# Kernel optimization log

Hardware: AMD Instinct MI355X
Metric: run time of the kernel (lower is better)

Reference implementation:

```python
import jax, jax.numpy as jnp
import numpy as np

N = 200_000   # nodes per component
E = 400_000   # directed edges per component
F_IN = 32     # raw node features
H = 96        # hidden_dim / GatedGraphConv out_channels
L = 6         # num_layers inside GatedGraphConv
B = 4096      # number of molecules (graphs) in batch
FC = 4 * H    # 384


def _gru_cell(m, h, w_ih, w_hh, b_ih, b_hh):
    # torch.nn.GRUCell math; w_* are [3H, H], b_* are [3H]
    gi = m @ w_ih.T + b_ih
    gh = h @ w_hh.T + b_hh
    i_r, i_z, i_n = jnp.split(gi, 3, axis=1)
    h_r, h_z, h_n = jnp.split(gh, 3, axis=1)
    r = jax.nn.sigmoid(i_r + h_r)
    z = jax.nn.sigmoid(i_z + h_z)
    n = jnp.tanh(i_n + r * h_n)
    return (1.0 - z) * n + z * h


def _gated_graph_conv(x, edge_index, W, w_ih, w_hh, b_ih, b_hh):
    n_nodes = x.shape[0]
    h = jnp.pad(x, ((0, 0), (0, H - x.shape[1])))  # pad features to H
    src, dst = edge_index[0], edge_index[1]        # message flows src -> dst
    for i in range(L):
        m = h @ W[i]                                # [N, H]
        agg = jax.ops.segment_sum(m[src], dst, num_segments=n_nodes)
        h = _gru_cell(agg, h, w_ih, w_hh, b_ih, b_hh)
    return h


def _pool_component(x, edge_index, batch, W, w_ih, w_hh, b_ih, b_hh):
    h = jax.nn.relu(_gated_graph_conv(x, edge_index, W, w_ih, w_hh, b_ih, b_hh))
    sums = jax.ops.segment_sum(h, batch, num_segments=B)
    cnt = jax.ops.segment_sum(jnp.ones((h.shape[0], 1), h.dtype), batch, num_segments=B)
    return sums / jnp.maximum(cnt, 1.0)            # global_mean_pool -> [B, H]


def setup_inputs() -> dict:
    key = jax.random.key(0)
    ks = jax.random.split(key, 16)
    d = {}
    for i in range(3):
        c = str(i + 1)
        kx, ke, kb = jax.random.split(ks[i], 3)
        d['x' + c] = jax.random.normal(kx, (N, F_IN), jnp.float32)
        d['edge_index' + c] = jax.random.randint(ke, (2, E), 0, N)
        d['batch' + c] = jnp.sort(jax.random.randint(kb, (N,), 0, B))
        kw = jax.random.split(ks[3 + i], 5)
        d['W' + c] = jax.random.normal(kw[0], (L, H, H), jnp.float32) * 0.05
        d['wih' + c] = jax.random.normal(kw[1], (3 * H, H), jnp.float32) * 0.05
        d['whh' + c] = jax.random.normal(kw[2], (3 * H, H), jnp.float32) * 0.05
        d['bih' + c] = jax.random.normal(kw[3], (3 * H,), jnp.float32) * 0.05
        d['bhh' + c] = jax.random.normal(kw[4], (3 * H,), jnp.float32) * 0.05
    kf = jax.random.split(ks[7], 6)
    d['fc1_w'] = jax.random.normal(kf[0], (FC, FC * 4), jnp.float32) * 0.05
    d['fc1_b'] = jnp.zeros((FC * 4,), jnp.float32)
    d['fc2_w'] = jax.random.normal(kf[1], (FC * 4, FC), jnp.float32) * 0.05
    d['fc2_b'] = jnp.zeros((FC,), jnp.float32)
    d['fc3_w'] = jax.random.normal(kf[2], (FC, 3), jnp.float32) * 0.05
    d['fc3_b'] = jnp.zeros((3,), jnp.float32)
    return d


def reference(x1, edge_index1, batch1, x2, edge_index2, batch2, x3, edge_index3, batch3,
              W1, wih1, whh1, bih1, bhh1,
              W2, wih2, whh2, bih2, bhh2,
              W3, wih3, whh3, bih3, bhh3,
              fc1_w, fc1_b, fc2_w, fc2_b, fc3_w, fc3_b):
    g1 = _pool_component(x1, edge_index1, batch1, W1, wih1, whh1, bih1, bhh1)
    g2 = _pool_component(x2, edge_index2, batch2, W2, wih2, whh2, bih2, bhh2)
    g3 = _pool_component(x3, edge_index3, batch3, W3, wih3, whh3, bih3, bhh3)
    xx = g1 * g2 * g3
    x = jnp.concatenate((g1, g2, g3, xx), axis=1)   # [B, 4H]
    x = jax.nn.relu(x @ fc1_w + fc1_b)              # dropout is identity (eval)
    x = jax.nn.relu(x @ fc2_w + fc2_b)
    return x @ fc3_w + fc3_b                        # [B, 3]
```

## Files before the change

### kernel.cpp

```cpp
#include <hip/hip_runtime.h>
#include <math.h>

#define NN_ 200000
#define EE_ 400000
#define HH  96
#define LL  6
#define BB  4096
#define NT_ 12500
#define SCAN_B 1024
#define NB_SCAN 196

typedef short s8v __attribute__((ext_vector_type(8)));
typedef float f4v __attribute__((ext_vector_type(4)));
typedef float f2v __attribute__((ext_vector_type(2)));

static inline int cdiv(int a, int b) { return (a + b - 1) / b; }

__device__ __forceinline__ float sigmoidf_(float x) { return 1.0f / (1.0f + __expf(-x)); }
__device__ __forceinline__ float tanhf_(float x) { return 1.0f - 2.0f / (__expf(2.0f * x) + 1.0f); }
__device__ __forceinline__ unsigned short f2bf(float x) {
    unsigned u = __float_as_uint(x);
    unsigned r = u + 0x7FFF + ((u >> 16) & 1);
    return (unsigned short)(r >> 16);
}
__device__ __forceinline__ float bf2f(unsigned short u) {
    return __uint_as_float(((unsigned)u) << 16);
}
__device__ __forceinline__ s8v load_bf8(const float* __restrict__ p) {
    float4 v0 = *(const float4*)p;
    float4 v1 = *(const float4*)(p + 4);
    s8v r;
    r[0] = (short)f2bf(v0.x); r[1] = (short)f2bf(v0.y);
    r[2] = (short)f2bf(v0.z); r[3] = (short)f2bf(v0.w);
    r[4] = (short)f2bf(v1.x); r[5] = (short)f2bf(v1.y);
    r[6] = (short)f2bf(v1.z); r[7] = (short)f2bf(v1.w);
    return r;
}

__device__ __forceinline__ void accu_(f2v& a, unsigned u) {
    a[0] += __uint_as_float(u << 16);
    a[1] += __uint_as_float(u & 0xFFFF0000u);
}
__device__ __forceinline__ void acc_row_(f2v* ag2, const uint4& u, int ks) {
    accu_(ag2[ks * 4 + 0], u.x); accu_(ag2[ks * 4 + 1], u.y);
    accu_(ag2[ks * 4 + 2], u.z); accu_(ag2[ks * 4 + 3], u.w);
}

__global__ void packB_k(const float* __restrict__ B, unsigned short* __restrict__ Bp,
                        int K, int N)
{
    int idx = blockIdx.x * 256 + threadIdx.x;
    if (idx >= K * N) return;
    int k = idx / N, n = idx % N;
    Bp[(((size_t)(k >> 5) * N + n) * 4 + ((k >> 3) & 3)) * 8 + (k & 7)] = f2bf(B[idx]);
}

__global__ void packWp_k(const float* __restrict__ W, unsigned short* __restrict__ Wp)
{
    int idx = blockIdx.x * 256 + threadIdx.x;
    if (idx >= LL * 6 * 3 * 64 * 8) return;
    int j    = idx & 7;
    int lane = (idx >> 3) & 63;
    int rest = idx >> 9;
    int ks = rest % 3;
    int jb = (rest / 3) % 6;
    int l  = rest / 18;
    int quad = lane >> 4, lc = lane & 15;
    int k = ks * 32 + quad * 8 + j;
    int n = jb * 16 + lc;
    Wp[idx] = f2bf(W[(size_t)l * 9216 + (size_t)k * 96 + n]);
}

__global__ void packWgc_k(const float* __restrict__ wih, const float* __restrict__ whh,
                          unsigned short* __restrict__ Wgc)
{
    int idx = blockIdx.x * 256 + threadIdx.x;
    if (idx >= 6 * 18 * 64 * 8) return;
    int j    = idx & 7;
    int lane = (idx >> 3) & 63;
    int rest = idx >> 9;
    int ksb = rest % 18;
    int jb  = rest / 18;
    int quad = lane >> 4, lc = lane & 15;
    int g, ks;
    if (ksb < 6)       { g = 0; ks = ksb; }
    else if (ksb < 12) { g = 1; ks = ksb - 6; }
    else if (ksb < 15) { g = 2; ks = ksb - 12; }
    else               { g = 3; ks = ksb - 12; }
    int k = ks * 32 + quad * 8 + j;
    int n = g * 96 + jb * 16 + lc;
    float v;
    if (n < 192) {
        v = (k < 96) ? wih[(size_t)n * 96 + k] : whh[(size_t)n * 96 + (k - 96)];
    } else if (n < 288) {
        int jj = n - 192;
        v = wih[(size_t)(192 + jj) * 96 + k];
    } else {
        int jj = n - 288;
        v = whh[(size_t)(192 + jj) * 96 + (k - 96)];
    }
    Wgc[idx] = f2bf(v);
}

__global__ void bpack_k(const float* __restrict__ bih, const float* __restrict__ bhh,
                        float* __restrict__ bs)
{
    int j = threadIdx.x;
    if (j >= 96) return;
    bs[j]        = bih[j] + bhh[j];
    bs[96 + j]   = bih[96 + j] + bhh[96 + j];
    bs[192 + j]  = bih[192 + j];
    bs[288 + j]  = bhh[192 + j];
}

__global__ void pad_k(const float* __restrict__ x, float* __restrict__ h,
                      unsigned short* __restrict__ hbf)
{
    int idx = blockIdx.x * 256 + threadIdx.x;
    if (idx >= NN_ * HH) return;
    int n = idx / HH, j = idx % HH;
    float v = (j < 32) ? x[n * 32 + j] : 0.f;
    h[idx] = v;
    hbf[idx] = f2bf(v);
}

__global__ void deg_k(const int* __restrict__ ei, int* __restrict__ deg)
{
    int e = blockIdx.x * 256 + threadIdx.x;
    if (e >= EE_) return;
    atomicAdd(&deg[ei[EE_ + e]], 1);
}

__global__ __launch_bounds__(SCAN_B) void scan1_k(
    const int* __restrict__ deg, int* __restrict__ rp, int* __restrict__ bsum)
{
    __shared__ int sh[SCAN_B];
    int i = blockIdx.x * SCAN_B + threadIdx.x;
    int v = (i < NN_) ? deg[i] : 0;
    sh[threadIdx.x] = v;
    __syncthreads();
    for (int off = 1; off < SCAN_B; off <<= 1) {
        int t = (threadIdx.x >= off) ? sh[threadIdx.x - off] : 0;
        __syncthreads();
        sh[threadIdx.x] += t;
        __syncthreads();
    }
    if (i < NN_) rp[i] = sh[threadIdx.x] - v;
    if (threadIdx.x == SCAN_B - 1) bsum[blockIdx.x] = sh[threadIdx.x];
}

__global__ __launch_bounds__(256) void scan2_k(int* __restrict__ bsum)
{
    __shared__ int sh[256];
    int v = (threadIdx.x < NB_SCAN) ? bsum[threadIdx.x] : 0;
    sh[threadIdx.x] = v;
    __syncthreads();
    for (int off = 1; off < 256; off <<= 1) {
        int t = (threadIdx.x >= off) ? sh[threadIdx.x - off] : 0;
        __syncthreads();
        sh[threadIdx.x] += t;
        __syncthreads();
    }
    if (threadIdx.x < NB_SCAN) bsum[threadIdx.x] = sh[threadIdx.x] - v;
}

__global__ void scan3_k(int* __restrict__ rp, const int* __restrict__ bsum,
                        int* __restrict__ cur)
{
    int i = blockIdx.x * 256 + threadIdx.x;
    if (i < NN_) {
        int r = rp[i] + bsum[i / SCAN_B];
        rp[i] = r;
        cur[i] = r;
    }
    if (i == 0) rp[NN_] = EE_;
}

__global__ void fill_k(const int* __restrict__ ei, int* __restrict__ cur,
                       int* __restrict__ srcs)
{
    int e = blockIdx.x * 256 + threadIdx.x;
    if (e >= EE_) return;
    int s = ei[e];
    int d = ei[EE_ + e];
    int pos = atomicAdd(&cur[d], 1);
    srcs[pos] = s * 192;
}

__global__ void brp_k(const int* __restrict__ bat, int* __restrict__ rpb)
{
    int i = blockIdx.x * 256 + threadIdx.x;
    if (i >= NN_) return;
    int b = bat[i];
    if (i == 0) {
        for (int q = 0; q <= b; q++) rpb[q] = 0;
    } else {
        int p = bat[i - 1];
        for (int q = p + 1; q <= b; q++) rpb[q] = i;
    }
    if (i == NN_ - 1) {
        for (int q = b + 1; q <= BB; q++) rpb[q] = NN_;
    }
}

__global__ __launch_bounds__(128) void agg_k(
    const int* __restrict__ rp, const int* __restrict__ srcs,
    const unsigned short* __restrict__ hbf,
    unsigned short* __restrict__ aggbf)
{
    int tid  = threadIdx.x;
    int wave = tid >> 6;
    int lane = tid & 63;
    int quad = lane >> 4;
    int lc   = lane & 15;
    int nT0  = blockIdx.x * 4 + wave * 2;

    const char* gbase = (const char*)hbf + quad * 16;

    #pragma unroll
    for (int t = 0; t < 2; t++) {
        int node = (nT0 + t) * 16 + lc;
        f2v ag2[12];
        #pragma unroll
        for (int i = 0; i < 12; i++) ag2[i] = (f2v){0.f, 0.f};
        int e = rp[node], e1 = rp[node + 1];
        for (; e < e1; e++) {
            const char* r = gbase + srcs[e];
            uint4 u0 = *(const uint4*)r;
            uint4 u1 = *(const uint4*)(r + 64);
            uint4 u2 = *(const uint4*)(r + 128);
            acc_row_(ag2, u0, 0); acc_row_(ag2, u1, 1); acc_row_(ag2, u2, 2);
        }
        #pragma unroll
        for (int ks = 0; ks < 3; ks++) {
            unsigned q0 = (unsigned)f2bf(ag2[ks * 4 + 0][0]) | ((unsigned)f2bf(ag2[ks * 4 + 0][1]) << 16);
            unsigned q1 = (unsigned)f2bf(ag2[ks * 4 + 1][0]) | ((unsigned)f2bf(ag2[ks * 4 + 1][1]) << 16);
            unsigned q2 = (unsigned)f2bf(ag2[ks * 4 + 2][0]) | ((unsigned)f2bf(ag2[ks * 4 + 2][1]) << 16);
            unsigned q3 = (unsigned)f2bf(ag2[ks * 4 + 3][0]) | ((unsigned)f2bf(ag2[ks * 4 + 3][1]) << 16);
            *(uint4*)(aggbf + (size_t)node * 96 + ks * 32 + quad * 8) =
                make_uint4(q0, q1, q2, q3);
        }
    }
}

__global__ __launch_bounds__(512, 2) void gru_k(
    const unsigned short* __restrict__ aggbf,
    const unsigned short* __restrict__ Wp,
    const unsigned short* __restrict__ Wgc,
    const float* __restrict__ bs,
    float* __restrict__ h,
    unsigned short* __restrict__ hbf)
{
    __shared__ unsigned short lw[55296];
    __shared__ unsigned short as_[8][32][36];
    int tid = threadIdx.x;

    {
        const uint4* src = (const uint4*)Wgc;
        uint4* dst = (uint4*)lw;
        #pragma unroll
        for (int it = 0; it < 14; it++) {
            int i = it * 512 + tid;
            if (i < 6912) dst[i] = src[i];
        }
    }
    __syncthreads();

    int wave = tid >> 6;
    int lane = tid & 63;
    int quad = lane >> 4;
    int lc   = lane & 15;
    int nT0  = blockIdx.x * 16 + wave * 2;

    bool val[2];
    val[0] = (nT0 + 0) < NT_;
    val[1] = (nT0 + 1) < NT_;

    s8v z8;
    #pragma unroll
    for (int q = 0; q < 8; q++) z8[q] = 0;

    s8v hg[2][3], dh[2][3];
    #pragma unroll
    for (int t = 0; t < 2; t++) {
        int node = (nT0 + t) * 16 + lc;
        #pragma unroll
        for (int ks = 0; ks < 3; ks++) {
            if (val[t]) {
                hg[t][ks] = *(const s8v*)(aggbf + (size_t)node * 96 + ks * 32 + quad * 8);
                dh[t][ks] = *(const s8v*)(hbf   + (size_t)node * 96 + ks * 32 + quad * 8);
            } else {
                hg[t][ks] = z8;
                dh[t][ks] = z8;
            }
        }
    }

    s8v d[2][6];
    #pragma unroll
    for (int kb = 0; kb < 3; kb++) {
        #pragma unroll
        for (int jj = 0; jj < 2; jj++) {
            int jb = kb * 2 + jj;
            f4v a1[2] = {};
            #pragma unroll
            for (int ks = 0; ks < 3; ks++) {
                s8v w = *(const s8v*)(Wp + ((size_t)(jb * 3 + ks) * 64 + lane) * 8);
                a1[0] = __builtin_amdgcn_mfma_f32_16x16x32_bf16(w, hg[0][ks], a1[0], 0, 0, 0);
                a1[1] = __builtin_amdgcn_mfma_f32_16x16x32_bf16(w, hg[1][ks], a1[1], 0, 0, 0);
            }
            #pragma unroll
            for (int t = 0; t < 2; t++) {
                unsigned short o0 = f2bf(a1[t][0]), o1 = f2bf(a1[t][1]);
                unsigned short o2 = f2bf(a1[t][2]), o3 = f2bf(a1[t][3]);
                *(uint2*)&as_[wave][t * 16 + lc][jj * 16 + quad * 4] =
                    make_uint2((unsigned)o0 | ((unsigned)o1 << 16),
                               (unsigned)o2 | ((unsigned)o3 << 16));
            }
        }
        #pragma unroll
        for (int t = 0; t < 2; t++)
            d[t][kb] = *(const s8v*)&as_[wave][t * 16 + lc][quad * 8];
    }
    #pragma unroll
    for (int t = 0; t < 2; t++) {
        d[t][3] = dh[t][0]; d[t][4] = dh[t][1]; d[t][5] = dh[t][2];
    }

    for (int jb = 0; jb < 6; jb++) {
        float4 hold[2];
        #pragma unroll
        for (int t = 0; t < 2; t++) {
            if (val[t])
                hold[t] = *(const float4*)(h + (size_t)((nT0 + t) * 16 + lc) * 96 + jb * 16 + quad * 4);
            else
                hold[t] = make_float4(0.f, 0.f, 0.f, 0.f);
        }
        f4v acc[2][4] = {};
        const unsigned short* wj = lw + (size_t)jb * 18 * 512 + (size_t)lane * 8;
        #pragma unroll
        for (int ks = 0; ks < 6; ks++) {
            s8v w = *(const s8v*)(wj + ks * 512);
            acc[0][0] = __builtin_amdgcn_mfma_f32_16x16x32_bf16(w, d[0][ks], acc[0][0], 0, 0, 0);
            acc[1][0] = __builtin_amdgcn_mfma_f32_16x16x32_bf16(w, d[1][ks], acc[1][0], 0, 0, 0);
        }
        #pragma unroll
        for (int ks = 0; ks < 6; ks++) {
            s8v w = *(const s8v*)(wj + (6 + ks) * 512);
            acc[0][1] = __builtin_amdgcn_mfma_f32_16x16x32_bf16(w, d[0][ks], acc[0][1], 0, 0, 0);
            acc[1][1] = __builtin_amdgcn_mfma_f32_16x16x32_bf16(w, d[1][ks], acc[1][1], 0, 0, 0);
        }
        #pragma unroll
        for (int ks = 0; ks < 6; ks++) {
            s8v w = *(const s8v*)(wj + (12 + ks) * 512);
            int g = (ks < 3) ? 2 : 3;
            acc[0][g] = __builtin_amdgcn_mfma_f32_16x16x32_bf16(w, d[0][ks], acc[0][g], 0, 0, 0);
            acc[1][g] = __builtin_amdgcn_mfma_f32_16x16x32_bf16(w, d[1][ks], acc[1][g], 0, 0, 0);
        }
        const float* bp = bs + jb * 16 + quad * 4;
        float4 br  = *(const float4*)(bp);
        float4 bz  = *(const float4*)(bp + 96);
        float4 bin = *(const float4*)(bp + 192);
        float4 bhn = *(const float4*)(bp + 288);
        float brv[4]  = {br.x, br.y, br.z, br.w};
        float bzv[4]  = {bz.x, bz.y, bz.z, bz.w};
        float binv[4] = {bin.x, bin.y, bin.z, bin.w};
        float bhnv[4] = {bhn.x, bhn.y, bhn.z, bhn.w};
        #pragma unroll
        for (int t = 0; t < 2; t++) {
            if (!val[t]) continue;
            int node = (nT0 + t) * 16 + lc;
            float hv[4] = {hold[t].x, hold[t].y, hold[t].z, hold[t].w};
            float out[4];
            #pragma unroll
            for (int i = 0; i < 4; i++) {
                float rg = sigmoidf_(acc[t][0][i] + brv[i]);
                float zg = sigmoidf_(acc[t][1][i] + bzv[i]);
                float nn = tanhf_(acc[t][2][i] + binv[i] + rg * (acc[t][3][i] + bhnv[i]));
                out[i] = (1.f - zg) * nn + zg * hv[i];
            }
            float* hp = h + (size_t)node * 96 + jb * 16 + quad * 4;
            *(float4*)hp = make_float4(out[0], out[1], out[2], out[3]);
            unsigned short q0 = f2bf(out[0]), q1 = f2bf(out[1]);
            unsigned short q2 = f2bf(out[2]), q3 = f2bf(out[3]);
            *(uint2*)(hbf + (size_t)node * 96 + jb * 16 + quad * 4) =
                make_uint2((unsigned)q0 | ((unsigned)q1 << 16),
                           (unsigned)q2 | ((unsigned)q3 << 16));
        }
    }
}

__global__ __launch_bounds__(128) void pool_csr_k(
    const float* __restrict__ h, const int* __restrict__ rpb, float* __restrict__ g)
{
    int b = blockIdx.x;
    int j = threadIdx.x;
    if (j >= 96) return;
    int n0 = rpb[b], n1 = rpb[b + 1];
    float s = 0.f;
    for (int n = n0; n < n1; n++) s += fmaxf(h[(size_t)n * 96 + j], 0.f);
    float c = (float)(n1 - n0);
    g[(size_t)b * 96 + j] = s / fmaxf(c, 1.f);
}

__global__ void feat_k(const float* __restrict__ g1, const float* __restrict__ g2,
                       const float* __restrict__ g3, float* __restrict__ feat)
{
    int idx = blockIdx.x * 256 + threadIdx.x;
    if (idx >= BB * HH) return;
    int b = idx / HH, j = idx % HH;
    float a = g1[idx], bb = g2[idx], c = g3[idx];
    float* f = feat + (size_t)b * 384;
    f[j]       = a;
    f[96 + j]  = bb;
    f[192 + j] = c;
    f[288 + j] = a * bb * c;
}

__global__ __launch_bounds__(256) void gemm_mlp_mfma(
    const float* __restrict__ A, const unsigned short* __restrict__ Bp,
    const float* __restrict__ bias, float* __restrict__ C,
    int K, int N, int doRelu)
{
    int wave = threadIdx.x >> 6;
    int lane = threadIdx.x & 63;
    int quad = lane >> 4;
    int lc   = lane & 15;
    int rowA = blockIdx.y * 64 + wave * 16 + lc;
    int colb = blockIdx.x * 128;

    f4v acc[8] = {};
    for (int ks = 0; ks < K / 32; ks++) {
        s8v a = load_bf8(A + (size_t)rowA * K + ks * 32 + quad * 8);
        #pragma unroll
        for (int t = 0; t < 8; t++) {
            int n = colb + t * 16 + lc;
            s8v b = *(const s8v*)(Bp + ((size_t)(ks * N + n) * 4 + quad) * 8);
            acc[t] = __builtin_amdgcn_mfma_f32_16x16x32_bf16(a, b, acc[t], 0, 0, 0);
        }
    }
    int rowD = blockIdx.y * 64 + wave * 16 + quad * 4;
    #pragma unroll
    for (int t = 0; t < 8; t++) {
        int n = colb + t * 16 + lc;
        float bv = bias[n];
        #pragma unroll
        for (int r = 0; r < 4; r++) {
            float v = acc[t][r] + bv;
            if (doRelu) v = fmaxf(v, 0.f);
            C[(size_t)(rowD + r) * N + n] = v;
        }
    }
}

__global__ __launch_bounds__(256) void fc3_k(const float* __restrict__ t2,
                                             const float* __restrict__ w,
                                             const float* __restrict__ bias,
                                             float* __restrict__ out)
{
    int wave = threadIdx.x >> 6;
    int lane = threadIdx.x & 63;
    int b = blockIdx.x * 4 + wave;
    const float* row = t2 + (size_t)b * 384;
    float a0 = 0.f, a1 = 0.f, a2 = 0.f;
    #pragma unroll
    for (int kk = 0; kk < 6; kk++) {
        int k = kk * 64 + lane;
        float x = row[k];
        a0 += x * w[k * 3 + 0];
        a1 += x * w[k * 3 + 1];
        a2 += x * w[k * 3 + 2];
    }
    #pragma unroll
    for (int off = 32; off > 0; off >>= 1) {
        a0 += __shfl_down(a0, off);
        a1 += __shfl_down(a1, off);
        a2 += __shfl_down(a2, off);
    }
    if (lane == 0) {
        out[b * 3 + 0] = a0 + bias[0];
        out[b * 3 + 1] = a1 + bias[1];
        out[b * 3 + 2] = a2 + bias[2];
    }
}

extern "C" void kernel_launch(void* const* d_in, const int* in_sizes, int n_in,
                              void* d_out, int out_size, void* d_ws, size_t ws_size,
                              hipStream_t stream)
{
    float* ws    = (float*)d_ws;
    float* h     = ws;
    float* hbfF  = h + (size_t)NN_ * HH;
    float* aggF  = hbfF + (size_t)NN_ * HH / 2;
    float* wpF   = aggF + (size_t)NN_ * HH / 2;
    float* wgpF  = wpF + 27648;
    float* fc1pF = wgpF + 36864;
    float* fc2pF = fc1pF + 294912;
    float* g3    = fc2pF + 294912;
    int*   rp    = (int*)(g3 + 3 * (size_t)BB * HH);
    int*   srcs  = rp + 200064;
    int*   deg   = srcs + 400000;
    int*   cur   = deg + 200000;
    int*   bsum  = cur + 200000;
    int*   rpb   = bsum + 256;
    float* bs    = (float*)(rpb + 4097) + 1;

    unsigned short* hbf  = (unsigned short*)hbfF;
    unsigned short* agg  = (unsigned short*)aggF;
    unsigned short* Wp   = (unsigned short*)wpF;
    unsigned short* Wgc  = (unsigned short*)wgpF;
    unsigned short* fc1p = (unsigned short*)fc1pF;
    unsigned short* fc2p = (unsigned short*)fc2pF;

    float* feat = h;
    float* t1   = h + 2 * 1024 * 1024;
    float* t2   = h + 9 * 1024 * 1024;

    for (int c = 0; c < 3; c++) {
        const float* x   = (const float*)d_in[c * 8 + 0];
        const int*   ei  = (const int*)  d_in[c * 8 + 1];
        const int*   bat = (const int*)  d_in[c * 8 + 2];
        const float* W   = (const float*)d_in[c * 8 + 3];
        const float* wih = (const float*)d_in[c * 8 + 4];
        const float* whh = (const float*)d_in[c * 8 + 5];
        const float* bih = (const float*)d_in[c * 8 + 6];
        const float* bhh = (const float*)d_in[c * 8 + 7];

        hipMemsetAsync(deg, 0, NN_ * sizeof(int), stream);
        deg_k<<<cdiv(EE_, 256), 256, 0, stream>>>(ei, deg);
        scan1_k<<<NB_SCAN, SCAN_B, 0, stream>>>(deg, rp, bsum);
        scan2_k<<<1, 256, 0, stream>>>(bsum);
        scan3_k<<<cdiv(NN_, 256), 256, 0, stream>>>(rp, bsum, cur);
        fill_k<<<cdiv(EE_, 256), 256, 0, stream>>>(ei, cur, srcs);
        brp_k<<<cdiv(NN_, 256), 256, 0, stream>>>(bat, rpb);

        packWp_k<<<cdiv(LL * 6 * 3 * 64 * 8, 256), 256, 0, stream>>>(W, Wp);
        packWgc_k<<<cdiv(6 * 18 * 64 * 8, 256), 256, 0, stream>>>(wih, whh, Wgc);
        bpack_k<<<1, 128, 0, stream>>>(bih, bhh, bs);
        pad_k<<<cdiv(NN_ * HH, 256), 256, 0, stream>>>(x, h, hbf);

        for (int l = 0; l < LL; l++) {
            agg_k<<<NN_ / 64, 128, 0, stream>>>(rp, srcs, hbf, agg);
            gru_k<<<cdiv(NT_, 16), 512, 0, stream>>>(
                agg, Wp + (size_t)l * 9216, Wgc, bs, h, hbf);
        }

        pool_csr_k<<<BB, 128, 0, stream>>>(h, rpb, g3 + (size_t)c * BB * HH);
    }

    const float* fc1_w = (const float*)d_in[24];
    const float* fc1_b = (const float*)d_in[25];
    const float* fc2_w = (const float*)d_in[26];
    const float* fc2_b = (const float*)d_in[27];
    const float* fc3_w = (const float*)d_in[28];
    const float* fc3_b = (const float*)d_in[29];

    packB_k<<<cdiv(384 * 1536, 256), 256, 0, stream>>>(fc1_w, fc1p, 384, 1536);
    packB_k<<<cdiv(1536 * 384, 256), 256, 0, stream>>>(fc2_w, fc2p, 1536, 384);

    feat_k<<<cdiv(BB * HH, 256), 256, 0, stream>>>(
        g3, g3 + (size_t)BB * HH, g3 + 2 * (size_t)BB * HH, feat);
    gemm_mlp_mfma<<<dim3(1536 / 128, BB / 64), 256, 0, stream>>>(
        feat, fc1p, fc1_b, t1, 384, 1536, 1);
    gemm_mlp_mfma<<<dim3(384 / 128, BB / 64), 256, 0, stream>>>(
        t1, fc2p, fc2_b, t2, 1536, 384, 1);
    fc3_k<<<BB / 4, 256, 0, stream>>>(t2, fc3_w, fc3_b, (float*)d_out);
}
```

Measured before the change: 2.822 ms.

## Split GRU output columns across two blocks, double-buffer bf16 hidden state, shrink MLP tiles

The GRU kernel now runs on a 2-D grid where each block computes half of the output gate columns. Each block loads only half of the gate weights into LDS, which halves shared memory use and drops the two-blocks-per-CU launch bound so occupancy can rise. The bf16 hidden state is double-buffered (ping-pong), so one block half can no longer overwrite state the other half is still reading. In exchange, both halves recompute the message matmul and reload the same input rows. The MLP GEMM tiles also shrink to 16 rows per block with each wave owning 32 columns, giving more blocks but less reuse of the A tile.

Result: faster. 2.710 ms (-4.0%).

```diff
diff --git a/kernel.cpp b/kernel.cpp
--- a/kernel.cpp
+++ b/kernel.cpp
@@ -243,25 +243,27 @@
     }
 }
 
-__global__ __launch_bounds__(512, 2) void gru_k(
+__global__ __launch_bounds__(512) void gru_k(
     const unsigned short* __restrict__ aggbf,
     const unsigned short* __restrict__ Wp,
     const unsigned short* __restrict__ Wgc,
     const float* __restrict__ bs,
     float* __restrict__ h,
-    unsigned short* __restrict__ hbf)
-{
-    __shared__ unsigned short lw[55296];
+    const unsigned short* __restrict__ hbf_prev,
+    unsigned short* __restrict__ hbf_next)
+{
+    __shared__ unsigned short lw[27648];
     __shared__ unsigned short as_[8][32][36];
-    int tid = threadIdx.x;
+    int tid  = threadIdx.x;
+    int half = blockIdx.y;
 
     {
-        const uint4* src = (const uint4*)Wgc;
+        const uint4* src = (const uint4*)Wgc + (size_t)half * 3456;
         uint4* dst = (uint4*)lw;
         #pragma unroll
-        for (int it = 0; it < 14; it++) {
+        for (int it = 0; it < 7; it++) {
             int i = it * 512 + tid;
-            if (i < 6912) dst[i] = src[i];
+            if (i < 3456) dst[i] = src[i];
         }
     }
     __syncthreads();
@@ -287,8 +289,8 @@
         #pragma unroll
         for (int ks = 0; ks < 3; ks++) {
             if (val[t]) {
-                hg[t][ks] = *(const s8v*)(aggbf + (size_t)node * 96 + ks * 32 + quad * 8);
-                dh[t][ks] = *(const s8v*)(hbf   + (size_t)node * 96 + ks * 32 + quad * 8);
+                hg[t][ks] = *(const s8v*)(aggbf    + (size_t)node * 96 + ks * 32 + quad * 8);
+                dh[t][ks] = *(const s8v*)(hbf_prev + (size_t)node * 96 + ks * 32 + quad * 8);
             } else {
                 hg[t][ks] = z8;
                 dh[t][ks] = z8;
@@ -327,7 +329,8 @@
         d[t][3] = dh[t][0]; d[t][4] = dh[t][1]; d[t][5] = dh[t][2];
     }
 
-    for (int jb = 0; jb < 6; jb++) {
+    for (int jbl = 0; jbl < 3; jbl++) {
+        int jb = half * 3 + jbl;
         float4 hold[2];
         #pragma unroll
         for (int t = 0; t < 2; t++) {
@@ -337,7 +340,7 @@
                 hold[t] = make_float4(0.f, 0.f, 0.f, 0.f);
         }
         f4v acc[2][4] = {};
-        const unsigned short* wj = lw + (size_t)jb * 18 * 512 + (size_t)lane * 8;
+        const unsigned short* wj = lw + (size_t)jbl * 18 * 512 + (size_t)lane * 8;
         #pragma unroll
         for (int ks = 0; ks < 6; ks++) {
             s8v w = *(const s8v*)(wj + ks * 512);
@@ -383,7 +386,7 @@
             *(float4*)hp = make_float4(out[0], out[1], out[2], out[3]);
             unsigned short q0 = f2bf(out[0]), q1 = f2bf(out[1]);
             unsigned short q2 = f2bf(out[2]), q3 = f2bf(out[3]);
-            *(uint2*)(hbf + (size_t)node * 96 + jb * 16 + quad * 4) =
+            *(uint2*)(hbf_next + (size_t)node * 96 + jb * 16 + quad * 4) =
                 make_uint2((unsigned)q0 | ((unsigned)q1 << 16),
                            (unsigned)q2 | ((unsigned)q3 << 16));
         }
@@ -426,22 +429,22 @@
     int lane = threadIdx.x & 63;
     int quad = lane >> 4;
     int lc   = lane & 15;
-    int rowA = blockIdx.y * 64 + wave * 16 + lc;
-    int colb = blockIdx.x * 128;
-
-    f4v acc[8] = {};
+    int rowA = blockIdx.y * 16 + lc;
+    int colb = blockIdx.x * 128 + wave * 32;
+
+    f4v acc[2] = {};
     for (int ks = 0; ks < K / 32; ks++) {
         s8v a = load_bf8(A + (size_t)rowA * K + ks * 32 + quad * 8);
         #pragma unroll
-        for (int t = 0; t < 8; t++) {
+        for (int t = 0; t < 2; t++) {
             int n = colb + t * 16 + lc;
             s8v b = *(const s8v*)(Bp + ((size_t)(ks * N + n) * 4 + quad) * 8);
             acc[t] = __builtin_amdgcn_mfma_f32_16x16x32_bf16(a, b, acc[t], 0, 0, 0);
         }
     }
-    int rowD = blockIdx.y * 64 + wave * 16 + quad * 4;
-    #pragma unroll
-    for (int t = 0; t < 8; t++) {
+    int rowD = blockIdx.y * 16 + quad * 4;
+    #pragma unroll
+    for (int t = 0; t < 2; t++) {
         int n = colb + t * 16 + lc;
         float bv = bias[n];
         #pragma unroll
@@ -490,8 +493,9 @@
 {
     float* ws    = (float*)d_ws;
     float* h     = ws;
-    float* hbfF  = h + (size_t)NN_ * HH;
-    float* aggF  = hbfF + (size_t)NN_ * HH / 2;
+    float* hbfAF = h + (size_t)NN_ * HH;
+    float* hbfBF = hbfAF + (size_t)NN_ * HH / 2;
+    float* aggF  = hbfBF + (size_t)NN_ * HH / 2;
     float* wpF   = aggF + (size_t)NN_ * HH / 2;
     float* wgpF  = wpF + 27648;
     float* fc1pF = wgpF + 36864;
@@ -505,7 +509,8 @@
     int*   rpb   = bsum + 256;
     float* bs    = (float*)(rpb + 4097) + 1;
 
-    unsigned short* hbf  = (unsigned short*)hbfF;
+    unsigned short* hbfA = (unsigned short*)hbfAF;
+    unsigned short* hbfB = (unsigned short*)hbfBF;
     unsigned short* agg  = (unsigned short*)aggF;
     unsigned short* Wp   = (unsigned short*)wpF;
     unsigned short* Wgc  = (unsigned short*)wgpF;
@@ -537,12 +542,13 @@
         packWp_k<<<cdiv(LL * 6 * 3 * 64 * 8, 256), 256, 0, stream>>>(W, Wp);
         packWgc_k<<<cdiv(6 * 18 * 64 * 8, 256), 256, 0, stream>>>(wih, whh, Wgc);
         bpack_k<<<1, 128, 0, stream>>>(bih, bhh, bs);
-        pad_k<<<cdiv(NN_ * HH, 256), 256, 0, stream>>>(x, h, hbf);
-
+        pad_k<<<cdiv(NN_ * HH, 256), 256, 0, stream>>>(x, h, hbfA);
+
+        unsigned short* pb[2] = {hbfA, hbfB};
         for (int l = 0; l < LL; l++) {
-            agg_k<<<NN_ / 64, 128, 0, stream>>>(rp, srcs, hbf, agg);
-            gru_k<<<cdiv(NT_, 16), 512, 0, stream>>>(
-                agg, Wp + (size_t)l * 9216, Wgc, bs, h, hbf);
+            agg_k<<<NN_ / 64, 128, 0, stream>>>(rp, srcs, pb[l & 1], agg);
+            gru_k<<<dim3(cdiv(NT_, 16), 2), 512, 0, stream>>>(
+                agg, Wp + (size_t)l * 9216, Wgc, bs, h, pb[l & 1], pb[(l + 1) & 1]);
         }
 
         pool_csr_k<<<BB, 128, 0, stream>>>(h, rpb, g3 + (size_t)c * BB * HH);
@@ -560,9 +566,9 @@
 
     feat_k<<<cdiv(BB * HH, 256), 256, 0, stream>>>(
         g3, g3 + (size_t)BB * HH, g3 + 2 * (size_t)BB * HH, feat);
-    gemm_mlp_mfma<<<dim3(1536 / 128, BB / 64), 256, 0, stream>>>(
+    gemm_mlp_mfma<<<dim3(1536 / 128, BB / 16), 256, 0, stream>>>(
         feat, fc1p, fc1_b, t1, 384, 1536, 1);
-    gemm_mlp_mfma<<<dim3(384 / 128, BB / 64), 256, 0, stream>>>(
+    gemm_mlp_mfma<<<dim3(384 / 128, BB / 16), 256, 0, stream>>>(
         t1, fc2p, fc2_b, t2, 1536, 384, 1);
     fc3_k<<<BB / 4, 256, 0, stream>>>(t2, fc3_w, fc3_b, (float*)d_out);
 }
```
